# Kernel optimization log

Measured on AMD Instinct MI355X. Metric: run time of the kernel, lower is better.

## Reference

```python
import jax, jax.numpy as jnp
import numpy as np
import math

H = 8  # num_heads

def _gelu(x):
    return jax.nn.gelu(x, approximate=False)

def setup_inputs() -> dict:
    key = jax.random.key(0)
    ks = jax.random.split(key, 16)
    B, N, T, D = 2, 16, 127, 128
    s = 0.02
    inp = {}
    inp["padded_batches"] = jax.random.normal(ks[0], (B, N, T, D), jnp.float32)
    inp["masks"] = jax.random.randint(ks[1], (B, N, T), 0, 2).astype(jnp.int32)
    inp["positions_3d"] = jax.random.normal(ks[2], (B, N, T, 3), jnp.float32)
    inp["Wq"] = jax.random.normal(ks[3], (D, D), jnp.float32) * s
    inp["bq"] = jnp.zeros((D,), jnp.float32)
    inp["Wk"] = jax.random.normal(ks[4], (D, D), jnp.float32) * s
    inp["bk"] = jnp.zeros((D,), jnp.float32)
    inp["Wv"] = jax.random.normal(ks[5], (D, D), jnp.float32) * s
    inp["bv"] = jnp.zeros((D,), jnp.float32)
    inp["gamma"] = jnp.ones((D,), jnp.float32)
    inp["beta"] = jnp.zeros((D,), jnp.float32)
    inp["token_embedding"] = jax.random.normal(ks[6], (1, D), jnp.float32)
    inp["Wb1"] = jax.random.normal(ks[7], (6, 64), jnp.float32) * s
    inp["bb1"] = jnp.zeros((64,), jnp.float32)
    inp["Wb2"] = jax.random.normal(ks[8], (64, H), jnp.float32) * s
    inp["bb2"] = jnp.zeros((H,), jnp.float32)
    inp["Wv1"] = jax.random.normal(ks[9], (6, 128), jnp.float32) * s
    inp["bv1"] = jnp.zeros((128,), jnp.float32)
    inp["Wv2"] = jax.random.normal(ks[10], (128, D), jnp.float32) * s
    inp["bv2"] = jnp.zeros((D,), jnp.float32)
    return inp

def reference(padded_batches, masks, positions_3d, Wq, bq, Wk, bk, Wv, bv, gamma, beta, token_embedding, Wb1, bb1, Wb2, bb2, Wv1, bv1, Wv2, bv2):
    B, N, T, D = padded_batches.shape
    Hd = D // H
    L = T + 1
    scale = 1.0 / math.sqrt(Hd)
    # prepend cls token
    cls = jnp.broadcast_to(token_embedding, (B, N, 1, D))
    x = jnp.concatenate([cls, padded_batches], axis=-2)  # [B,N,L,D]
    q = (x @ Wq + bq).reshape(B * N, L, H, Hd).transpose(0, 2, 1, 3)
    k = (x @ Wk + bk).reshape(B * N, L, H, Hd).transpose(0, 2, 1, 3)
    v = (x @ Wv + bv).reshape(B * N, L, H, Hd).transpose(0, 2, 1, 3)
    keep = jnp.concatenate([jnp.ones((B, N, 1), masks.dtype), masks], axis=-1)
    large_neg = jnp.finfo(jnp.float32).min
    key_mask = jnp.where(keep == 0, large_neg, 0.0).astype(jnp.float32).reshape(B * N, 1, 1, L)
    logits = jnp.einsum('bhid,bhjd->bhij', q, k) * scale
    # relative positional features
    pos = jnp.concatenate([jnp.zeros((B, N, 1, 3), positions_3d.dtype), positions_3d], axis=-2).reshape(B * N, L, 3)
    diff = pos[:, :, None, :] - pos[:, None, :, :]  # [BN,L,L,3]
    dist2 = jnp.sum(diff ** 2, axis=-1, keepdims=True)
    dist = jnp.sqrt(dist2)
    rel_feat = jnp.concatenate([diff, dist, dist, dist2], axis=-1)  # [BN,L,L,6]
    rel_bias = (_gelu(rel_feat @ Wb1 + bb1) @ Wb2 + bb2).transpose(0, 3, 1, 2)  # [BN,H,L,L]
    rel_bias = rel_bias.at[:, :, 0, :].set(0.0).at[:, :, :, 0].set(0.0)
    logits = logits + rel_bias + key_mask
    w = jax.nn.softmax(logits, axis=-1)
    attn = jnp.einsum('bhij,bhjd->bhid', w, v)
    rel_val = (_gelu(rel_feat @ Wv1 + bv1) @ Wv2 + bv2).reshape(B * N, L, L, H, Hd).transpose(0, 3, 1, 2, 4)
    rel_val = rel_val.at[:, :, 0, :, :].set(0.0).at[:, :, :, 0, :].set(0.0)
    attn = attn + jnp.einsum('bhij,bhijc->bhic', w, rel_val)
    attn = attn.transpose(0, 2, 1, 3).reshape(B, N, L, D)
    st = attn[:, :, :1, :] + x[:, :, :1, :]
    mu = jnp.mean(st, axis=-1, keepdims=True)
    var = jnp.var(st, axis=-1, keepdims=True)
    sum_token = (st - mu) / jnp.sqrt(var + 1e-5) * gamma + beta
    out = attn[:, :, 1:, :] + x[:, :, 1:, :]
    return (out, sum_token)
```

## Files before the change

### kernel.cpp

```cpp
#include <hip/hip_runtime.h>
#include <hip/hip_bf16.h>
#include <math.h>

#define BN 32
#define L 128
#define D 128
#define TT 127
#define NH 8

typedef float f32x4 __attribute__((ext_vector_type(4)));
typedef short s16x8 __attribute__((ext_vector_type(8)));

__device__ __forceinline__ float gelu_sig(float x) {
    float e = __expf(-1.702f * x);
    return x * __builtin_amdgcn_rcpf(1.0f + e);
}
__device__ __forceinline__ unsigned short f2bf(float f) {
    unsigned u = __float_as_uint(f);
    return (unsigned short)((u + 0x7fffu + ((u >> 16) & 1u)) >> 16);
}
__device__ __forceinline__ float bf2f(unsigned short v) {
    return __uint_as_float((unsigned)v << 16);
}

__global__ __launch_bounds__(256)
void qkv_kernel(const float* __restrict__ padded, const float* __restrict__ tok,
                const float* __restrict__ Wq, const float* __restrict__ bq,
                const float* __restrict__ Wk, const float* __restrict__ bk,
                const float* __restrict__ Wv, const float* __restrict__ bv,
                const float* __restrict__ Wb1, const float* __restrict__ bb1,
                const float* __restrict__ Wb2,
                const float* __restrict__ Wv1, const float* __restrict__ bv1,
                const float* __restrict__ Wv2,
                float* __restrict__ Qo, float* __restrict__ Ko, float* __restrict__ Vo,
                float* __restrict__ CW, float* __restrict__ RVW,
                unsigned short* __restrict__ WV2F) {
    const int s = blockIdx.x;
    const int mat = blockIdx.y;
    const int chunk = blockIdx.z;
    const float* W = (mat == 0) ? Wq : (mat == 1) ? Wk : Wv;
    const float* bias = (mat == 0) ? bq : (mat == 1) ? bk : bv;
    float* outp = (mat == 0) ? Qo : (mat == 1) ? Ko : Vo;

    __shared__ unsigned short Xs[32][136];
    const int tid = threadIdx.x;

    {
        const int row = tid >> 3;
        const int colbase = (tid & 7) * 16;
        const int i = chunk * 32 + row;
        const float* src = (i == 0) ? tok : &padded[(size_t)s * TT * D + (size_t)(i - 1) * D];
#pragma unroll
        for (int k4 = 0; k4 < 4; ++k4) {
            float4 v = *(const float4*)&src[colbase + k4 * 4];
            unsigned lo = (unsigned)f2bf(v.x) | ((unsigned)f2bf(v.y) << 16);
            unsigned hi = (unsigned)f2bf(v.z) | ((unsigned)f2bf(v.w) << 16);
            *(uint2*)&Xs[row][colbase + k4 * 4] = make_uint2(lo, hi);
        }
    }
    __syncthreads();

    const int wave = tid >> 6;
    const int lane = tid & 63;
    const int hA = lane & 15;
    const int kg = lane >> 4;

    s16x8 afr[2][4];
#pragma unroll
    for (int m = 0; m < 2; ++m)
#pragma unroll
        for (int kt = 0; kt < 4; ++kt)
            afr[m][kt] = *(const s16x8*)&Xs[m * 16 + hA][kt * 32 + kg * 8];

    f32x4 acc[2][2];
#pragma unroll
    for (int m = 0; m < 2; ++m)
#pragma unroll
        for (int n = 0; n < 2; ++n) acc[m][n] = (f32x4){0.f, 0.f, 0.f, 0.f};

#pragma unroll
    for (int kt = 0; kt < 4; ++kt) {
#pragma unroll
        for (int n = 0; n < 2; ++n) {
            const int col = (2 * wave + n) * 16 + hA;
            s16x8 bw;
#pragma unroll
            for (int e = 0; e < 8; ++e)
                bw[e] = (short)f2bf(W[(size_t)(kt * 32 + kg * 8 + e) * D + col]);
            acc[0][n] = __builtin_amdgcn_mfma_f32_16x16x32_bf16(afr[0][kt], bw, acc[0][n], 0, 0, 0);
            acc[1][n] = __builtin_amdgcn_mfma_f32_16x16x32_bf16(afr[1][kt], bw, acc[1][n], 0, 0, 0);
        }
    }

#pragma unroll
    for (int n = 0; n < 2; ++n) {
        const int col = (2 * wave + n) * 16 + hA;
        const float bc = bias[col];
#pragma unroll
        for (int m = 0; m < 2; ++m)
#pragma unroll
            for (int r = 0; r < 4; ++r) {
                const int row = chunk * 32 + m * 16 + kg * 4 + r;
                outp[(size_t)s * L * D + (size_t)row * D + col] = acc[m][n][r] + bc;
            }
    }

    if (s == 0 && mat == 0 && chunk == 0) {
        if (tid < 64) {
            const int u = tid;
            CW[u * 16 + 0] = Wb1[0 * 64 + u];
            CW[u * 16 + 1] = Wb1[1 * 64 + u];
            CW[u * 16 + 2] = Wb1[2 * 64 + u];
            CW[u * 16 + 3] = Wb1[3 * 64 + u] + Wb1[4 * 64 + u];
            CW[u * 16 + 4] = Wb1[5 * 64 + u];
            CW[u * 16 + 5] = bb1[u];
            CW[u * 16 + 6] = 0.f;
            CW[u * 16 + 7] = 0.f;
#pragma unroll
            for (int k = 0; k < 8; ++k) CW[u * 16 + 8 + k] = Wb2[u * 8 + k];
        }
        if (tid < 128) {
            const int cc = tid;
            RVW[cc * 8 + 0] = Wv1[0 * 128 + cc];
            RVW[cc * 8 + 1] = Wv1[1 * 128 + cc];
            RVW[cc * 8 + 2] = Wv1[2 * 128 + cc];
            RVW[cc * 8 + 3] = Wv1[3 * 128 + cc] + Wv1[4 * 128 + cc];
            RVW[cc * 8 + 4] = Wv1[5 * 128 + cc];
            RVW[cc * 8 + 5] = bv1[cc];
            RVW[cc * 8 + 6] = 0.f;
            RVW[cc * 8 + 7] = 0.f;
        }
        for (int idx = tid; idx < 16384; idx += 256) {
            int f = idx >> 9, r = idx & 511, ln = r >> 3, e = r & 7;
            int kt = f >> 3, ng = f & 7;
            int row = kt * 32 + (ln >> 4) * 8 + e;
            int col = ng * 16 + (ln & 15);
            WV2F[idx] = f2bf(Wv2[(size_t)row * D + col]);
        }
    }
}

__global__ __launch_bounds__(256)
void logits_kernel(const float* __restrict__ Q, const float* __restrict__ K,
                   __hip_bfloat16* __restrict__ LW) {
    const int s = blockIdx.x;
    const int h = blockIdx.y;
    const int tid = threadIdx.x;
    const int wv = tid >> 6;
    const int lane = tid & 63;
    const int lrn = lane & 15;
    const int kg = lane >> 4;

    __shared__ float Qs[128][16];
    __shared__ float Ks[128][16];
    for (int e = tid; e < 2048; e += 256) {
        int i = e >> 4, d = e & 15;
        Qs[i][d] = Q[((size_t)s * L + i) * D + h * 16 + d];
        Ks[i][d] = K[((size_t)s * L + i) * D + h * 16 + d];
    }
    __syncthreads();

    s16x8 afr[2];
#pragma unroll
    for (int m = 0; m < 2; ++m) {
        s16x8 a;
#pragma unroll
        for (int e = 0; e < 8; ++e) a[e] = 0;
        if (kg < 2) {
            const int i = wv * 32 + m * 16 + lrn;
            float4 q0 = *(const float4*)&Qs[i][kg * 8];
            float4 q1 = *(const float4*)&Qs[i][kg * 8 + 4];
            a[0] = (short)f2bf(q0.x); a[1] = (short)f2bf(q0.y);
            a[2] = (short)f2bf(q0.z); a[3] = (short)f2bf(q0.w);
            a[4] = (short)f2bf(q1.x); a[5] = (short)f2bf(q1.y);
            a[6] = (short)f2bf(q1.z); a[7] = (short)f2bf(q1.w);
        }
        afr[m] = a;
    }

    __hip_bfloat16* lw = LW + ((size_t)(s * NH + h) * L) * L;
#pragma unroll
    for (int n = 0; n < 8; ++n) {
        s16x8 b;
#pragma unroll
        for (int e = 0; e < 8; ++e) b[e] = 0;
        if (kg < 2) {
            const int j = n * 16 + lrn;
            float4 k0 = *(const float4*)&Ks[j][kg * 8];
            float4 k1 = *(const float4*)&Ks[j][kg * 8 + 4];
            b[0] = (short)f2bf(k0.x); b[1] = (short)f2bf(k0.y);
            b[2] = (short)f2bf(k0.z); b[3] = (short)f2bf(k0.w);
            b[4] = (short)f2bf(k1.x); b[5] = (short)f2bf(k1.y);
            b[6] = (short)f2bf(k1.z); b[7] = (short)f2bf(k1.w);
        }
#pragma unroll
        for (int m = 0; m < 2; ++m) {
            f32x4 acc = (f32x4){0.f, 0.f, 0.f, 0.f};
            acc = __builtin_amdgcn_mfma_f32_16x16x32_bf16(afr[m], b, acc, 0, 0, 0);
#pragma unroll
            for (int r = 0; r < 4; ++r)
                lw[(size_t)(wv * 32 + m * 16 + kg * 4 + r) * L + n * 16 + lrn] =
                    __float2bfloat16(acc[r] * 0.25f);
        }
    }
}

__global__ __launch_bounds__(256)
void bias_kernel(const float* __restrict__ pos3d, const float* __restrict__ CW,
                 const float* __restrict__ bb2, __hip_bfloat16* __restrict__ LW) {
    const int bid = blockIdx.x;
    const int s = bid >> 6;
    const int pair = (bid & 63) * 256 + threadIdx.x;
    const int i = pair >> 7;
    const int j = pair & 127;
    if (i == 0 || j == 0) return;

    const float* pi = pos3d + ((size_t)s * TT + (i - 1)) * 3;
    const float* pj = pos3d + ((size_t)s * TT + (j - 1)) * 3;
    const float dx = pi[0] - pj[0], dy = pi[1] - pj[1], dz = pi[2] - pj[2];
    const float dist2 = dx * dx + dy * dy + dz * dz;
    const float dist = sqrtf(dist2);

    float bias[NH];
#pragma unroll
    for (int hh = 0; hh < NH; ++hh) bias[hh] = 0.f;
    const float4* cw4 = (const float4*)CW;
#pragma unroll 2
    for (int u = 0; u < 64; ++u) {
        float4 wa  = cw4[u * 4 + 0];
        float4 wb  = cw4[u * 4 + 1];
        float4 w2a = cw4[u * 4 + 2];
        float4 w2b = cw4[u * 4 + 3];
        float hv = wb.y;
        hv = fmaf(dx, wa.x, hv);
        hv = fmaf(dy, wa.y, hv);
        hv = fmaf(dz, wa.z, hv);
        hv = fmaf(dist, wa.w, hv);
        hv = fmaf(dist2, wb.x, hv);
        hv = gelu_sig(hv);
        bias[0] = fmaf(hv, w2a.x, bias[0]);
        bias[1] = fmaf(hv, w2a.y, bias[1]);
        bias[2] = fmaf(hv, w2a.z, bias[2]);
        bias[3] = fmaf(hv, w2a.w, bias[3]);
        bias[4] = fmaf(hv, w2b.x, bias[4]);
        bias[5] = fmaf(hv, w2b.y, bias[5]);
        bias[6] = fmaf(hv, w2b.z, bias[6]);
        bias[7] = fmaf(hv, w2b.w, bias[7]);
    }
#pragma unroll
    for (int hh = 0; hh < NH; ++hh) {
        const size_t o = ((size_t)(s * NH + hh) * L + i) * L + j;
        LW[o] = __float2bfloat16(__bfloat162float(LW[o]) + bias[hh] + bb2[hh]);
    }
}

__global__ __launch_bounds__(256, 4)
void attn_kernel(const float* __restrict__ padded, const int* __restrict__ masks,
                 const float* __restrict__ pos3d,
                 const float* __restrict__ gamma, const float* __restrict__ beta,
                 const float* __restrict__ tok,
                 const float* __restrict__ RVW,
                 const unsigned short* __restrict__ WV2F,
                 const float* __restrict__ bv2,
                 const float* __restrict__ V, const __hip_bfloat16* __restrict__ LW,
                 float* __restrict__ out) {
    const int i = blockIdx.x;
    const int s = blockIdx.y;
    const int tid = threadIdx.x;
    const int wave = tid >> 6;
    const int lane = tid & 63;
    const int hA = lane & 15;
    const int kg = lane >> 4;
    const int j = tid & 127;
    const int hbase = (tid >> 7) * 4;

    __shared__ float4 feat4_lds[144];
    __shared__ float  feat5_lds[L];
    __shared__ unsigned short w_bf[NH][136];
    __shared__ unsigned short gs_bf[NH][136];
    __shared__ float  a1_part[8][132];
    __shared__ float  a2_lds[D];
    __shared__ float  reds[4][NH];
    __shared__ float  red2[2][2];
    __shared__ unsigned long long kb_lds[2];
    __shared__ int    jmap_lds[128];

    __hip_bfloat16 lr4[4];
#pragma unroll
    for (int k = 0; k < 4; ++k)
        lr4[k] = LW[((size_t)(s * NH + hbase + k) * L + i) * L + j];
    const int keep = (j == 0) ? 1 : masks[(size_t)s * TT + (j - 1)];

    const unsigned long long bal = __ballot(keep != 0);
    if (lane == 0 && wave < 2) kb_lds[wave] = bal;

    if (tid < 128) {
        float pix = 0.f, piy = 0.f, piz = 0.f;
        if (i > 0) { const float* pp = pos3d + ((size_t)s * TT + (i - 1)) * 3; pix = pp[0]; piy = pp[1]; piz = pp[2]; }
        float pjx = 0.f, pjy = 0.f, pjz = 0.f;
        if (tid > 0) { const float* pp = pos3d + ((size_t)s * TT + (tid - 1)) * 3; pjx = pp[0]; pjy = pp[1]; pjz = pp[2]; }
        const float dx = pix - pjx, dy = piy - pjy, dz = piz - pjz;
        const float dist2 = dx * dx + dy * dy + dz * dz;
        const float dist = sqrtf(dist2);
        feat4_lds[tid + (tid >> 3)] = make_float4(dx, dy, dz, dist);
        feat5_lds[tid] = dist2;
        jmap_lds[tid] = 0;
    }
    for (int idx = tid; idx < NH * 68; idx += 256) ((unsigned*)w_bf)[idx] = 0u;
    __syncthreads();

    const unsigned long long b0 = kb_lds[0];
    const int nk = __popcll(b0) + __popcll(kb_lds[1]);
    const int NK32 = (nk + 31) >> 5;
    int rank = 0;
    if (keep) {
        rank = __popcll(bal & ((1ull << lane) - 1)) + ((wave & 1) ? __popcll(b0) : 0);
        if (wave < 2) jmap_lds[rank] = j;
    }

    float p4[4];
#pragma unroll
    for (int k = 0; k < 4; ++k) {
        float lv = __bfloat162float(lr4[k]);
        p4[k] = keep ? __expf(lv) : 0.f;
    }
#pragma unroll
    for (int k = 0; k < 4; ++k) {
        float v = p4[k];
        for (int off = 32; off >= 1; off >>= 1) v += __shfl_xor(v, off, 64);
        if (lane == 0) reds[wave][hbase + k] = v;
    }
    __syncthreads();
    if (keep) {
        const int pb = (tid >> 7) * 2;
#pragma unroll
        for (int k = 0; k < 4; ++k) {
            const int hh = hbase + k;
            float inv = __builtin_amdgcn_rcpf(reds[pb][hh] + reds[pb + 1][hh]);
            w_bf[hh][rank] = f2bf(p4[k] * inv);
        }
    }
    __syncthreads();

    const int jg = tid >> 5;
    const int c0v = (tid & 31) * 4;
    const int h0v = c0v >> 4;
    const int perg = NK32 * 4;
    const float* Vs = V + (size_t)s * L * D;

    if (i > 0) {
        const int ng0 = 2 * wave;
        float rvw[2][6];
#pragma unroll
        for (int n = 0; n < 2; ++n) {
            const int c = (ng0 + n) * 16 + hA;
            float4 ra = *(const float4*)&RVW[(size_t)c * 8 + 0];
            rvw[n][0] = ra.x; rvw[n][1] = ra.y; rvw[n][2] = ra.z; rvw[n][3] = ra.w;
            rvw[n][4] = RVW[(size_t)c * 8 + 4];
            rvw[n][5] = RVW[(size_t)c * 8 + 5];
        }

        f32x4 accG[2];
#pragma unroll
        for (int n = 0; n < 2; ++n) accG[n] = (f32x4){0.f, 0.f, 0.f, 0.f};

#pragma unroll
        for (int kt = 0; kt < 4; ++kt) {
            if (kt >= NK32) break;
            s16x8 wf;
#pragma unroll
            for (int e = 0; e < 8; ++e) wf[e] = 0;
            if (hA < NH) {
                wf = *(const s16x8*)&w_bf[hA][kt * 32 + kg * 8];
                if (kt == 0 && kg == 0) wf[0] = 0;
            }
            s16x8 bfr[2];
#pragma unroll
            for (int e = 0; e < 8; ++e) {
                const int jj = jmap_lds[kt * 32 + kg * 8 + e];
                float4 fa = feat4_lds[jj + (jj >> 3)];
                float f5 = feat5_lds[jj];
#pragma unroll
                for (int n = 0; n < 2; ++n) {
                    float hv = rvw[n][5];
                    hv = fmaf(fa.x, rvw[n][0], hv);
                    hv = fmaf(fa.y, rvw[n][1], hv);
                    hv = fmaf(fa.z, rvw[n][2], hv);
                    hv = fmaf(fa.w, rvw[n][3], hv);
                    hv = fmaf(f5,  rvw[n][4], hv);
                    bfr[n][e] = (short)f2bf(gelu_sig(hv));
                }
            }
#pragma unroll
            for (int n = 0; n < 2; ++n)
                accG[n] = __builtin_amdgcn_mfma_f32_16x16x32_bf16(wf, bfr[n], accG[n], 0, 0, 0);
        }

        float a1a[4] = {0.f, 0.f, 0.f, 0.f};
        for (int r = 0; r < perg; ++r) {
            const int jt = jg * perg + r;
            const int jr = jmap_lds[jt];
            float4 vcur = *(const float4*)&Vs[(size_t)jr * D + c0v];
            const float wj = bf2f(w_bf[h0v][jt]);
            a1a[0] = fmaf(wj, vcur.x, a1a[0]);
            a1a[1] = fmaf(wj, vcur.y, a1a[1]);
            a1a[2] = fmaf(wj, vcur.z, a1a[2]);
            a1a[3] = fmaf(wj, vcur.w, a1a[3]);
        }
        *(float4*)&a1_part[jg][c0v] = make_float4(a1a[0], a1a[1], a1a[2], a1a[3]);

        if (lane < 32) {
#pragma unroll
            for (int n = 0; n < 2; ++n)
#pragma unroll
                for (int r = 0; r < 4; ++r)
                    gs_bf[(lane >> 4) * 4 + r][(ng0 + n) * 16 + hA] = f2bf(accG[n][r]);
        }
        __syncthreads();

        f32x4 acc2[2];
#pragma unroll
        for (int n = 0; n < 2; ++n) acc2[n] = (f32x4){0.f, 0.f, 0.f, 0.f};
#pragma unroll
        for (int kt = 0; kt < 4; ++kt) {
            s16x8 gf;
#pragma unroll
            for (int e = 0; e < 8; ++e) gf[e] = 0;
            if (hA < NH)
                gf = *(const s16x8*)&gs_bf[hA][kt * 32 + kg * 8];
#pragma unroll
            for (int n = 0; n < 2; ++n) {
                const int f = kt * 8 + ng0 + n;
                s16x8 bw = *(const s16x8*)&WV2F[((size_t)f * 64 + lane) * 8];
                acc2[n] = __builtin_amdgcn_mfma_f32_16x16x32_bf16(gf, bw, acc2[n], 0, 0, 0);
            }
        }
#pragma unroll
        for (int n = 0; n < 2; ++n) {
            const int f = ng0 + n;
            if (kg == (f >> 2)) a2_lds[f * 16 + hA] = acc2[n][f & 3];
        }
        __syncthreads();

        if (tid < 128) {
            float a1f = a1_part[0][tid] + a1_part[1][tid] + a1_part[2][tid] + a1_part[3][tid]
                      + a1_part[4][tid] + a1_part[5][tid] + a1_part[6][tid] + a1_part[7][tid];
            const float S1 = 1.0f - bf2f(w_bf[tid >> 4][0]);
            const size_t o = (size_t)s * TT * D + (size_t)(i - 1) * D + tid;
            out[o] = a1f + a2_lds[tid] + S1 * bv2[tid] + padded[o];
        }
    } else {
        float a1a[4] = {0.f, 0.f, 0.f, 0.f};
        for (int r = 0; r < perg; ++r) {
            const int jt = jg * perg + r;
            const int jr = jmap_lds[jt];
            float4 vcur = *(const float4*)&Vs[(size_t)jr * D + c0v];
            const float wj = bf2f(w_bf[h0v][jt]);
            a1a[0] = fmaf(wj, vcur.x, a1a[0]);
            a1a[1] = fmaf(wj, vcur.y, a1a[1]);
            a1a[2] = fmaf(wj, vcur.z, a1a[2]);
            a1a[3] = fmaf(wj, vcur.w, a1a[3]);
        }
        *(float4*)&a1_part[jg][c0v] = make_float4(a1a[0], a1a[1], a1a[2], a1a[3]);
        __syncthreads();

        float st = 0.f;
        if (tid < 128) {
            float a1f = a1_part[0][tid] + a1_part[1][tid] + a1_part[2][tid] + a1_part[3][tid]
                      + a1_part[4][tid] + a1_part[5][tid] + a1_part[6][tid] + a1_part[7][tid];
            st = a1f + tok[tid];
            float sum = st, sum2 = st * st;
            for (int off = 32; off >= 1; off >>= 1) {
                sum += __shfl_xor(sum, off, 64);
                sum2 += __shfl_xor(sum2, off, 64);
            }
            if (lane == 0) { red2[wave][0] = sum; red2[wave][1] = sum2; }
        }
        __syncthreads();
        if (tid < 128) {
            float sum = red2[0][0] + red2[1][0];
            float sum2 = red2[0][1] + red2[1][1];
            const float mu = sum * (1.0f / 128.0f);
            const float var = sum2 * (1.0f / 128.0f) - mu * mu;
            const float y = (st - mu) * rsqrtf(var + 1e-5f) * gamma[tid] + beta[tid];
            out[(size_t)BN * TT * D + (size_t)s * D + tid] = y;
        }
    }
}

extern "C" void kernel_launch(void* const* d_in, const int* in_sizes, int n_in,
                              void* d_out, int out_size, void* d_ws, size_t ws_size,
                              hipStream_t stream) {
    const float* padded = (const float*)d_in[0];
    const int*   masks  = (const int*)d_in[1];
    const float* pos3d  = (const float*)d_in[2];
    const float* Wq = (const float*)d_in[3];
    const float* bq = (const float*)d_in[4];
    const float* Wk = (const float*)d_in[5];
    const float* bk = (const float*)d_in[6];
    const float* Wv = (const float*)d_in[7];
    const float* bv = (const float*)d_in[8];
    const float* gamma = (const float*)d_in[9];
    const float* beta  = (const float*)d_in[10];
    const float* tok   = (const float*)d_in[11];
    const float* Wb1 = (const float*)d_in[12];
    const float* bb1 = (const float*)d_in[13];
    const float* Wb2 = (const float*)d_in[14];
    const float* bb2 = (const float*)d_in[15];
    const float* Wv1 = (const float*)d_in[16];
    const float* bv1 = (const float*)d_in[17];
    const float* Wv2 = (const float*)d_in[18];
    const float* bv2 = (const float*)d_in[19];
    float* out = (float*)d_out;

    float* Q  = (float*)d_ws;
    float* K  = Q + (size_t)BN * L * D;
    float* Vw = K + (size_t)BN * L * D;
    __hip_bfloat16* LW = (__hip_bfloat16*)(Vw + (size_t)BN * L * D);
    float* CW  = (float*)(LW + (size_t)BN * NH * L * L);
    float* RVW = CW + 64 * 16;
    unsigned short* WV2F = (unsigned short*)(RVW + 128 * 8);

    qkv_kernel<<<dim3(BN, 3, 4), 256, 0, stream>>>(padded, tok, Wq, bq, Wk, bk, Wv, bv,
                                                   Wb1, bb1, Wb2, Wv1, bv1, Wv2,
                                                   Q, K, Vw, CW, RVW, WV2F);
    logits_kernel<<<dim3(BN, NH), 256, 0, stream>>>(Q, K, LW);
    bias_kernel<<<dim3(2048), 256, 0, stream>>>(pos3d, CW, bb2, LW);
    attn_kernel<<<dim3(L, BN), 256, 0, stream>>>(padded, masks, pos3d, gamma, beta, tok,
                                                 RVW, WV2F, bv2,
                                                 Vw, LW, out);
}
```

Baseline: 82.86 us.

## Merge logits and bias kernels into one launch with separate bias buffer

Combines the QK logits kernel and the relative-position bias kernel into a single launch whose blocks split by index range, so the two run concurrently instead of serially. The bias now goes to its own packed bf16 buffer laid out per (s,j,i) with 8 heads contiguous, written as one 16-byte store. The attention kernel adds it when it loads the logits. Bias work is also skipped for masked keys, which removes the read-modify-write of LW and one launch. The cost is an extra workspace buffer and a second global read in attn_kernel.

```diff
diff --git a/kernel.cpp b/kernel.cpp
--- a/kernel.cpp
+++ b/kernel.cpp
@@ -141,116 +141,126 @@
 }
 
 __global__ __launch_bounds__(256)
-void logits_kernel(const float* __restrict__ Q, const float* __restrict__ K,
-                   __hip_bfloat16* __restrict__ LW) {
-    const int s = blockIdx.x;
-    const int h = blockIdx.y;
+void mid_kernel(const float* __restrict__ Q, const float* __restrict__ K,
+                const int* __restrict__ masks,
+                const float* __restrict__ pos3d, const float* __restrict__ CW,
+                const float* __restrict__ bb2,
+                __hip_bfloat16* __restrict__ LW, unsigned short* __restrict__ BIAS) {
+    const int bid = blockIdx.x;
     const int tid = threadIdx.x;
-    const int wv = tid >> 6;
-    const int lane = tid & 63;
-    const int lrn = lane & 15;
-    const int kg = lane >> 4;
 
     __shared__ float Qs[128][16];
     __shared__ float Ks[128][16];
-    for (int e = tid; e < 2048; e += 256) {
-        int i = e >> 4, d = e & 15;
-        Qs[i][d] = Q[((size_t)s * L + i) * D + h * 16 + d];
-        Ks[i][d] = K[((size_t)s * L + i) * D + h * 16 + d];
-    }
-    __syncthreads();
-
-    s16x8 afr[2];
-#pragma unroll
-    for (int m = 0; m < 2; ++m) {
-        s16x8 a;
-#pragma unroll
-        for (int e = 0; e < 8; ++e) a[e] = 0;
-        if (kg < 2) {
-            const int i = wv * 32 + m * 16 + lrn;
-            float4 q0 = *(const float4*)&Qs[i][kg * 8];
-            float4 q1 = *(const float4*)&Qs[i][kg * 8 + 4];
-            a[0] = (short)f2bf(q0.x); a[1] = (short)f2bf(q0.y);
-            a[2] = (short)f2bf(q0.z); a[3] = (short)f2bf(q0.w);
-            a[4] = (short)f2bf(q1.x); a[5] = (short)f2bf(q1.y);
-            a[6] = (short)f2bf(q1.z); a[7] = (short)f2bf(q1.w);
-        }
-        afr[m] = a;
-    }
-
-    __hip_bfloat16* lw = LW + ((size_t)(s * NH + h) * L) * L;
-#pragma unroll
-    for (int n = 0; n < 8; ++n) {
-        s16x8 b;
-#pragma unroll
-        for (int e = 0; e < 8; ++e) b[e] = 0;
-        if (kg < 2) {
-            const int j = n * 16 + lrn;
-            float4 k0 = *(const float4*)&Ks[j][kg * 8];
-            float4 k1 = *(const float4*)&Ks[j][kg * 8 + 4];
-            b[0] = (short)f2bf(k0.x); b[1] = (short)f2bf(k0.y);
-            b[2] = (short)f2bf(k0.z); b[3] = (short)f2bf(k0.w);
-            b[4] = (short)f2bf(k1.x); b[5] = (short)f2bf(k1.y);
-            b[6] = (short)f2bf(k1.z); b[7] = (short)f2bf(k1.w);
-        }
+
+    if (bid < 256) {
+        const int s = bid >> 3;
+        const int h = bid & 7;
+        const int wv = tid >> 6;
+        const int lane = tid & 63;
+        const int lrn = lane & 15;
+        const int kg = lane >> 4;
+
+        for (int e = tid; e < 2048; e += 256) {
+            int i = e >> 4, d = e & 15;
+            Qs[i][d] = Q[((size_t)s * L + i) * D + h * 16 + d];
+            Ks[i][d] = K[((size_t)s * L + i) * D + h * 16 + d];
+        }
+        __syncthreads();
+
+        s16x8 afr[2];
 #pragma unroll
         for (int m = 0; m < 2; ++m) {
-            f32x4 acc = (f32x4){0.f, 0.f, 0.f, 0.f};
-            acc = __builtin_amdgcn_mfma_f32_16x16x32_bf16(afr[m], b, acc, 0, 0, 0);
-#pragma unroll
-            for (int r = 0; r < 4; ++r)
-                lw[(size_t)(wv * 32 + m * 16 + kg * 4 + r) * L + n * 16 + lrn] =
-                    __float2bfloat16(acc[r] * 0.25f);
-        }
-    }
-}
-
-__global__ __launch_bounds__(256)
-void bias_kernel(const float* __restrict__ pos3d, const float* __restrict__ CW,
-                 const float* __restrict__ bb2, __hip_bfloat16* __restrict__ LW) {
-    const int bid = blockIdx.x;
-    const int s = bid >> 6;
-    const int pair = (bid & 63) * 256 + threadIdx.x;
-    const int i = pair >> 7;
-    const int j = pair & 127;
-    if (i == 0 || j == 0) return;
-
-    const float* pi = pos3d + ((size_t)s * TT + (i - 1)) * 3;
-    const float* pj = pos3d + ((size_t)s * TT + (j - 1)) * 3;
-    const float dx = pi[0] - pj[0], dy = pi[1] - pj[1], dz = pi[2] - pj[2];
-    const float dist2 = dx * dx + dy * dy + dz * dz;
-    const float dist = sqrtf(dist2);
-
-    float bias[NH];
-#pragma unroll
-    for (int hh = 0; hh < NH; ++hh) bias[hh] = 0.f;
-    const float4* cw4 = (const float4*)CW;
+            s16x8 a;
+#pragma unroll
+            for (int e = 0; e < 8; ++e) a[e] = 0;
+            if (kg < 2) {
+                const int i = wv * 32 + m * 16 + lrn;
+                float4 q0 = *(const float4*)&Qs[i][kg * 8];
+                float4 q1 = *(const float4*)&Qs[i][kg * 8 + 4];
+                a[0] = (short)f2bf(q0.x); a[1] = (short)f2bf(q0.y);
+                a[2] = (short)f2bf(q0.z); a[3] = (short)f2bf(q0.w);
+                a[4] = (short)f2bf(q1.x); a[5] = (short)f2bf(q1.y);
+                a[6] = (short)f2bf(q1.z); a[7] = (short)f2bf(q1.w);
+            }
+            afr[m] = a;
+        }
+
+        __hip_bfloat16* lw = LW + ((size_t)(s * NH + h) * L) * L;
+#pragma unroll
+        for (int n = 0; n < 8; ++n) {
+            s16x8 b;
+#pragma unroll
+            for (int e = 0; e < 8; ++e) b[e] = 0;
+            if (kg < 2) {
+                const int j = n * 16 + lrn;
+                float4 k0 = *(const float4*)&Ks[j][kg * 8];
+                float4 k1 = *(const float4*)&Ks[j][kg * 8 + 4];
+                b[0] = (short)f2bf(k0.x); b[1] = (short)f2bf(k0.y);
+                b[2] = (short)f2bf(k0.z); b[3] = (short)f2bf(k0.w);
+                b[4] = (short)f2bf(k1.x); b[5] = (short)f2bf(k1.y);
+                b[6] = (short)f2bf(k1.z); b[7] = (short)f2bf(k1.w);
+            }
+#pragma unroll
+            for (int m = 0; m < 2; ++m) {
+                f32x4 acc = (f32x4){0.f, 0.f, 0.f, 0.f};
+                acc = __builtin_amdgcn_mfma_f32_16x16x32_bf16(afr[m], b, acc, 0, 0, 0);
+#pragma unroll
+                for (int r = 0; r < 4; ++r)
+                    lw[(size_t)(wv * 32 + m * 16 + kg * 4 + r) * L + n * 16 + lrn] =
+                        __float2bfloat16(acc[r] * 0.25f);
+            }
+        }
+    } else {
+        const int b2 = bid - 256;
+        const int s = b2 >> 6;
+        const int jp = b2 & 63;
+        const int wv = tid >> 6;
+        const int lane = tid & 63;
+        const int j = jp * 2 + (wv >> 1);
+        const int i = (wv & 1) * 64 + lane;
+
+        if (j == 0) return;
+        if (!masks[(size_t)s * TT + (j - 1)]) return;
+        if (i == 0) return;
+
+        const float* pi = pos3d + ((size_t)s * TT + (i - 1)) * 3;
+        const float* pj = pos3d + ((size_t)s * TT + (j - 1)) * 3;
+        const float dx = pi[0] - pj[0], dy = pi[1] - pj[1], dz = pi[2] - pj[2];
+        const float dist2 = dx * dx + dy * dy + dz * dz;
+        const float dist = sqrtf(dist2);
+
+        float bias[NH];
+#pragma unroll
+        for (int hh = 0; hh < NH; ++hh) bias[hh] = 0.f;
+        const float4* cw4 = (const float4*)CW;
 #pragma unroll 2
-    for (int u = 0; u < 64; ++u) {
-        float4 wa  = cw4[u * 4 + 0];
-        float4 wb  = cw4[u * 4 + 1];
-        float4 w2a = cw4[u * 4 + 2];
-        float4 w2b = cw4[u * 4 + 3];
-        float hv = wb.y;
-        hv = fmaf(dx, wa.x, hv);
-        hv = fmaf(dy, wa.y, hv);
-        hv = fmaf(dz, wa.z, hv);
-        hv = fmaf(dist, wa.w, hv);
-        hv = fmaf(dist2, wb.x, hv);
-        hv = gelu_sig(hv);
-        bias[0] = fmaf(hv, w2a.x, bias[0]);
-        bias[1] = fmaf(hv, w2a.y, bias[1]);
-        bias[2] = fmaf(hv, w2a.z, bias[2]);
-        bias[3] = fmaf(hv, w2a.w, bias[3]);
-        bias[4] = fmaf(hv, w2b.x, bias[4]);
-        bias[5] = fmaf(hv, w2b.y, bias[5]);
-        bias[6] = fmaf(hv, w2b.z, bias[6]);
-        bias[7] = fmaf(hv, w2b.w, bias[7]);
-    }
-#pragma unroll
-    for (int hh = 0; hh < NH; ++hh) {
-        const size_t o = ((size_t)(s * NH + hh) * L + i) * L + j;
-        LW[o] = __float2bfloat16(__bfloat162float(LW[o]) + bias[hh] + bb2[hh]);
+        for (int u = 0; u < 64; ++u) {
+            float4 wa  = cw4[u * 4 + 0];
+            float4 wb  = cw4[u * 4 + 1];
+            float4 w2a = cw4[u * 4 + 2];
+            float4 w2b = cw4[u * 4 + 3];
+            float hv = wb.y;
+            hv = fmaf(dx, wa.x, hv);
+            hv = fmaf(dy, wa.y, hv);
+            hv = fmaf(dz, wa.z, hv);
+            hv = fmaf(dist, wa.w, hv);
+            hv = fmaf(dist2, wb.x, hv);
+            hv = gelu_sig(hv);
+            bias[0] = fmaf(hv, w2a.x, bias[0]);
+            bias[1] = fmaf(hv, w2a.y, bias[1]);
+            bias[2] = fmaf(hv, w2a.z, bias[2]);
+            bias[3] = fmaf(hv, w2a.w, bias[3]);
+            bias[4] = fmaf(hv, w2b.x, bias[4]);
+            bias[5] = fmaf(hv, w2b.y, bias[5]);
+            bias[6] = fmaf(hv, w2b.z, bias[6]);
+            bias[7] = fmaf(hv, w2b.w, bias[7]);
+        }
+        uint4 ow;
+        ow.x = (unsigned)f2bf(bias[0] + bb2[0]) | ((unsigned)f2bf(bias[1] + bb2[1]) << 16);
+        ow.y = (unsigned)f2bf(bias[2] + bb2[2]) | ((unsigned)f2bf(bias[3] + bb2[3]) << 16);
+        ow.z = (unsigned)f2bf(bias[4] + bb2[4]) | ((unsigned)f2bf(bias[5] + bb2[5]) << 16);
+        ow.w = (unsigned)f2bf(bias[6] + bb2[6]) | ((unsigned)f2bf(bias[7] + bb2[7]) << 16);
+        *(uint4*)&BIAS[(((size_t)s * L + j) * L + i) * 8] = ow;
     }
 }
 
@@ -263,6 +273,7 @@
                  const unsigned short* __restrict__ WV2F,
                  const float* __restrict__ bv2,
                  const float* __restrict__ V, const __hip_bfloat16* __restrict__ LW,
+                 const unsigned short* __restrict__ BIAS,
                  float* __restrict__ out) {
     const int i = blockIdx.x;
     const int s = blockIdx.y;
@@ -290,6 +301,9 @@
     for (int k = 0; k < 4; ++k)
         lr4[k] = LW[((size_t)(s * NH + hbase + k) * L + i) * L + j];
     const int keep = (j == 0) ? 1 : masks[(size_t)s * TT + (j - 1)];
+    const int ub = (i > 0) && (j > 0) && keep;
+    uint2 braw = make_uint2(0u, 0u);
+    if (ub) braw = *(const uint2*)&BIAS[(((size_t)s * L + j) * L + i) * 8 + hbase];
 
     const unsigned long long bal = __ballot(keep != 0);
     if (lane == 0 && wave < 2) kb_lds[wave] = bal;
@@ -318,10 +332,15 @@
         if (wave < 2) jmap_lds[rank] = j;
     }
 
+    float badd[4];
+    badd[0] = bf2f((unsigned short)(braw.x & 0xffffu));
+    badd[1] = bf2f((unsigned short)(braw.x >> 16));
+    badd[2] = bf2f((unsigned short)(braw.y & 0xffffu));
+    badd[3] = bf2f((unsigned short)(braw.y >> 16));
     float p4[4];
 #pragma unroll
     for (int k = 0; k < 4; ++k) {
-        float lv = __bfloat162float(lr4[k]);
+        float lv = __bfloat162float(lr4[k]) + badd[k];
         p4[k] = keep ? __expf(lv) : 0.f;
     }
 #pragma unroll
@@ -517,16 +536,16 @@
     float* K  = Q + (size_t)BN * L * D;
     float* Vw = K + (size_t)BN * L * D;
     __hip_bfloat16* LW = (__hip_bfloat16*)(Vw + (size_t)BN * L * D);
-    float* CW  = (float*)(LW + (size_t)BN * NH * L * L);
+    unsigned short* BIAS = (unsigned short*)(LW + (size_t)BN * NH * L * L);
+    float* CW  = (float*)(BIAS + (size_t)BN * L * L * NH);
     float* RVW = CW + 64 * 16;
     unsigned short* WV2F = (unsigned short*)(RVW + 128 * 8);
 
     qkv_kernel<<<dim3(BN, 3, 4), 256, 0, stream>>>(padded, tok, Wq, bq, Wk, bk, Wv, bv,
                                                    Wb1, bb1, Wb2, Wv1, bv1, Wv2,
                                                    Q, K, Vw, CW, RVW, WV2F);
-    logits_kernel<<<dim3(BN, NH), 256, 0, stream>>>(Q, K, LW);
-    bias_kernel<<<dim3(2048), 256, 0, stream>>>(pos3d, CW, bb2, LW);
+    mid_kernel<<<dim3(256 + BN * 64), 256, 0, stream>>>(Q, K, masks, pos3d, CW, bb2, LW, BIAS);
     attn_kernel<<<dim3(L, BN), 256, 0, stream>>>(padded, masks, pos3d, gamma, beta, tok,
                                                  RVW, WV2F, bv2,
-                                                 Vw, LW, out);
-}
+                                                 Vw, LW, BIAS, out);
+}
```

Result: faster. 79.10 us (-4.5%).
